# Performance work log

Hardware: AMD Instinct MI355X
Metric: run time of the kernel (lower is better)

Reference implementation:

```python
import jax, jax.numpy as jnp
import numpy as np

B, T, S, D, V = 32, 2048, 256, 1024, 56
STAR_PENALTY = -1.0
NEG = -1e30  # -inf surrogate that is safe for gradients


def setup_inputs() -> dict:
    key = jax.random.key(0)
    k1, k2, k3 = jax.random.split(key, 3)
    features = jax.random.normal(k1, (B, T, D), jnp.float32)
    targets = jax.random.randint(k2, (B, S), 1, V)  # 0 is the blank; labels in [1, V)
    W = jax.random.normal(k3, (V, D), jnp.float32) * (1.0 / 32.0)  # 1/sqrt(D)
    b = jnp.zeros((V,), jnp.float32)
    input_lengths = jnp.full((B,), T, jnp.int32)
    target_lengths = jnp.full((B,), S, jnp.int32)
    return dict(features=features, W=W, b=b, targets=targets,
                input_lengths=input_lengths, target_lengths=target_lengths)


def _star_ctc_losses(logp, targets, input_lengths, target_lengths, star_penalty):
    """Star-CTC forward (DP) score.
    logp: (T, N, C) log-softmax emissions; targets: (N, S) labels (blank=0 excluded).
    Extended state sequence [*, t1, *, t2, ..., tS, *]: star states play the role of
    CTC blanks but act as penalized wildcards, emitting logsumexp(logp)+star_penalty
    (== star_penalty for normalized log-probs). Standard CTC transition topology:
    self-loop, advance by 1, advance by 2 into a token state when it differs from the
    previous token. Returns per-sequence negative log-likelihood, shape (N,)."""
    Tlen, N, C = logp.shape
    Slen = targets.shape[1]
    L = 2 * Slen + 1
    ext = jnp.zeros((N, L), targets.dtype).at[:, 1::2].set(targets)  # (N, L)
    is_star = (jnp.arange(L) % 2 == 0)[None, :]                      # (1, L)
    prev2 = jnp.pad(ext[:, :-2], ((0, 0), (2, 0)), constant_values=-1)
    allow_skip = (~is_star) & (ext != prev2)                         # (N, L)

    def emit(logp_t):  # logp_t: (N, C) -> (N, L)
        star_e = star_penalty + jax.nn.logsumexp(logp_t, axis=-1, keepdims=True)
        tok_e = jnp.take_along_axis(logp_t, ext, axis=-1)
        return jnp.where(is_star, star_e, tok_e)

    alpha0 = jnp.where(jnp.arange(L)[None, :] < 2, emit(logp[0]), NEG)

    def step(alpha, xs):
        logp_t, t = xs
        a1 = jnp.pad(alpha[:, :-1], ((0, 0), (1, 0)), constant_values=NEG)
        a2 = jnp.where(allow_skip,
                       jnp.pad(alpha[:, :-2], ((0, 0), (2, 0)), constant_values=NEG),
                       NEG)
        new = jnp.logaddexp(jnp.logaddexp(alpha, a1), a2) + emit(logp_t)
        new = jnp.where(t < input_lengths[:, None], new, alpha)  # freeze past input_length
        return new, None

    alpha, _ = jax.lax.scan(step, alpha0, (logp[1:], jnp.arange(1, Tlen)))
    last = 2 * target_lengths                  # index of the final star state
    rows = jnp.arange(N)
    score = jnp.logaddexp(alpha[rows, last], alpha[rows, last - 1])
    return -score


def reference(features, W, b, targets, input_lengths, target_lengths):
    # classifier + log_softmax (Dropout(0.2) is identity at eval time)
    logits = jnp.einsum('btd,vd->btv', features, W) + b
    logp = jax.nn.log_softmax(logits.astype(jnp.float32), axis=-1)
    logp = jnp.transpose(logp, (1, 0, 2))      # (T, N, C) as in logits.permute(1,0,2)
    losses = _star_ctc_losses(logp, targets, input_lengths, target_lengths, STAR_PENALTY)
    # ctc_reduce_mean: length-normalized mean loss
    return jnp.mean(losses / target_lengths.astype(losses.dtype))
```

## Files before the change

### kernel.cpp

```cpp
#include <hip/hip_runtime.h>
#include <hip/hip_bf16.h>
#include <math.h>

typedef __attribute__((ext_vector_type(4))) float f32x4;
typedef __attribute__((ext_vector_type(8))) short s16x8;

#define LOG2E 1.4426950408889634f
#define LN2f  0.6931471805599453f
#define INV_E 0.36787944117144233f

__device__ __forceinline__ short bfc(float x) {
  unsigned u = __float_as_uint(x);
  unsigned r = u + 0x7fffu + ((u >> 16) & 1u);
  return (short)(r >> 16);
}

__device__ __forceinline__ unsigned pk2(float x, float y) {
  union { __hip_bfloat162 h; unsigned u; } c;
  c.h = __float22bfloat162_rn(make_float2(x, y));
  return c.u;
}

__device__ __forceinline__ float bperm(float v, int byte_addr) {
  return __int_as_float(__builtin_amdgcn_ds_bpermute(byte_addr, __float_as_int(v)));
}

__device__ __forceinline__ float rdlane(float v, int lane) {
  return __int_as_float(__builtin_amdgcn_readlane(__float_as_int(v), lane));
}

__device__ __forceinline__ float pick9(int j, float a0, float a1, float a2,
                                       float a3, float a4, float a5, float a6,
                                       float a7, float a8) {
  float v = a0;
  if (j == 1) v = a1;
  if (j == 2) v = a2;
  if (j == 3) v = a3;
  if (j == 4) v = a4;
  if (j == 5) v = a5;
  if (j == 6) v = a6;
  if (j == 7) v = a7;
  if (j == 8) v = a8;
  return v;
}

__global__ void conv_w(const float* __restrict__ W, short* __restrict__ Wb,
                       int V, int D) {
  int idx = blockIdx.x * blockDim.x + threadIdx.x;
  if (idx >= 64 * D) return;
  int row = idx / D, col = idx - row * D;
  Wb[idx] = (row < V) ? bfc(W[(size_t)row * D + col]) : (short)0;
}

__global__ __launch_bounds__(256) void fused_gemm_star(
    const float* __restrict__ feat, const short* __restrict__ Wb,
    const float* __restrict__ bias, float* __restrict__ pt,
    int* __restrict__ flags,
    const int* __restrict__ targets, const int* __restrict__ in_len,
    const int* __restrict__ tgt_len, float* __restrict__ partial,
    int nrows, int D, int V, int T, int S, int B, int CPB) {

  if ((int)blockIdx.x >= B) {
    const int j = blockIdx.x - B;
    const int b = j % B;
    const int c = j / B;
    const int tc0 = c * 128;
    const int rlen = (T - tc0 < 128) ? (T - tc0) : 128;
    const int rowlim = b * T + tc0 + rlen;

    const int lane = threadIdx.x & 63;
    const int wave = threadIdx.x >> 6;
    const int m_lo = lane & 15;
    const int q = lane >> 4;
    const int rowbase = b * T + tc0 + wave * 32;

    int arow0 = rowbase + m_lo;
    int arow1 = rowbase + 16 + m_lo;
    if (arow0 >= nrows) arow0 = nrows - 1;
    if (arow1 >= nrows) arow1 = nrows - 1;
    const float* Ap0 = feat + (size_t)arow0 * D + q * 8;
    const float* Ap1 = feat + (size_t)arow1 * D + q * 8;
    const short* Bp = Wb + (size_t)m_lo * D + q * 8;
    const size_t bstr = (size_t)16 * D;

    f32x4 acc[2][4];
    #pragma unroll
    for (int g = 0; g < 2; ++g)
      #pragma unroll
      for (int ni = 0; ni < 4; ++ni) acc[g][ni] = (f32x4){0.f, 0.f, 0.f, 0.f};

    float4 al0 = *(const float4*)(Ap0);
    float4 ah0 = *(const float4*)(Ap0 + 4);
    float4 al1 = *(const float4*)(Ap1);
    float4 ah1 = *(const float4*)(Ap1 + 4);
    s16x8 b0 = *(const s16x8*)(Bp);
    s16x8 b1 = *(const s16x8*)(Bp + bstr);
    s16x8 b2 = *(const s16x8*)(Bp + 2 * bstr);
    s16x8 b3 = *(const s16x8*)(Bp + 3 * bstr);

    for (int k0 = 0; k0 < D; k0 += 32) {
      const int kn = (k0 + 32 < D) ? (k0 + 32) : 0;
      const float* Ap0n = feat + (size_t)arow0 * D + kn + q * 8;
      const float* Ap1n = feat + (size_t)arow1 * D + kn + q * 8;
      const short* Bpn = Wb + (size_t)m_lo * D + kn + q * 8;
      float4 nal0 = *(const float4*)(Ap0n);
      float4 nah0 = *(const float4*)(Ap0n + 4);
      float4 nal1 = *(const float4*)(Ap1n);
      float4 nah1 = *(const float4*)(Ap1n + 4);
      s16x8 nb0 = *(const s16x8*)(Bpn);
      s16x8 nb1 = *(const s16x8*)(Bpn + bstr);
      s16x8 nb2 = *(const s16x8*)(Bpn + 2 * bstr);
      s16x8 nb3 = *(const s16x8*)(Bpn + 3 * bstr);

      union { s16x8 v; unsigned u[4]; } av0, av1;
      av0.u[0] = pk2(al0.x, al0.y); av0.u[1] = pk2(al0.z, al0.w);
      av0.u[2] = pk2(ah0.x, ah0.y); av0.u[3] = pk2(ah0.z, ah0.w);
      av1.u[0] = pk2(al1.x, al1.y); av1.u[1] = pk2(al1.z, al1.w);
      av1.u[2] = pk2(ah1.x, ah1.y); av1.u[3] = pk2(ah1.z, ah1.w);

      acc[0][0] = __builtin_amdgcn_mfma_f32_16x16x32_bf16(av0.v, b0, acc[0][0], 0, 0, 0);
      acc[0][1] = __builtin_amdgcn_mfma_f32_16x16x32_bf16(av0.v, b1, acc[0][1], 0, 0, 0);
      acc[0][2] = __builtin_amdgcn_mfma_f32_16x16x32_bf16(av0.v, b2, acc[0][2], 0, 0, 0);
      acc[0][3] = __builtin_amdgcn_mfma_f32_16x16x32_bf16(av0.v, b3, acc[0][3], 0, 0, 0);
      acc[1][0] = __builtin_amdgcn_mfma_f32_16x16x32_bf16(av1.v, b0, acc[1][0], 0, 0, 0);
      acc[1][1] = __builtin_amdgcn_mfma_f32_16x16x32_bf16(av1.v, b1, acc[1][1], 0, 0, 0);
      acc[1][2] = __builtin_amdgcn_mfma_f32_16x16x32_bf16(av1.v, b2, acc[1][2], 0, 0, 0);
      acc[1][3] = __builtin_amdgcn_mfma_f32_16x16x32_bf16(av1.v, b3, acc[1][3], 0, 0, 0);

      al0 = nal0; ah0 = nah0; al1 = nal1; ah1 = nah1;
      b0 = nb0; b1 = nb1; b2 = nb2; b3 = nb3;
    }

    float bias_v[4];
    #pragma unroll
    for (int ni = 0; ni < 4; ++ni) {
      int col = ni * 16 + m_lo;
      bias_v[ni] = (col < V) ? bias[col] : 0.f;
    }

    #pragma unroll
    for (int g = 0; g < 2; ++g) {
      #pragma unroll
      for (int r = 0; r < 4; ++r) {
        int grow = rowbase + g * 16 + q * 4 + r;
        float lg[4];
        #pragma unroll
        for (int ni = 0; ni < 4; ++ni) {
          int col = ni * 16 + m_lo;
          lg[ni] = (col < V) ? (acc[g][ni][r] + bias_v[ni]) : -1e30f;
        }
        float m = fmaxf(fmaxf(lg[0], lg[1]), fmaxf(lg[2], lg[3]));
        #pragma unroll
        for (int off = 1; off < 16; off <<= 1) m = fmaxf(m, __shfl_xor(m, off));
        float p[4];
        #pragma unroll
        for (int ni = 0; ni < 4; ++ni) p[ni] = exp2f((lg[ni] - m) * LOG2E);
        float s = (p[0] + p[1]) + (p[2] + p[3]);
        #pragma unroll
        for (int off = 1; off < 16; off <<= 1) s += __shfl_xor(s, off);

        if (grow < rowlim) {
          float* orow = pt + (size_t)grow * 64;
          orow[m_lo] = p[0];
          orow[16 + m_lo] = p[1];
          orow[32 + m_lo] = p[2];
          if (m_lo < 8)       orow[48 + m_lo] = p[3];
          else if (m_lo == 8) orow[56] = logf(s);
          else if (m_lo == 9) orow[57] = s * INV_E;
          else                orow[48 + m_lo] = 0.f;
        }
      }
    }

    __syncthreads();
    if (threadIdx.x == 0)
      __hip_atomic_store(&flags[b * CPB + c], 1, __ATOMIC_RELEASE,
                         __HIP_MEMORY_SCOPE_AGENT);
    return;
  }

  if (threadIdx.x >= 64) return;
  const int n = blockIdx.x;
  const int lane = threadIdx.x;
  const float* row = pt + (size_t)n * T * 64;
  const int len = in_len[n];
  const int tl = tgt_len[n];
  const int* tg = targets + (size_t)n * S;
  const int* fl = flags + n * CPB;

  int cdone = -1;
#define WAITC(cc)                                                            \
  do {                                                                       \
    int _c = (cc);                                                           \
    while (cdone < _c) {                                                     \
      if (__hip_atomic_load((int*)&fl[cdone + 1], __ATOMIC_ACQUIRE,          \
                            __HIP_MEMORY_SCOPE_AGENT))                       \
        ++cdone;                                                             \
      else                                                                   \
        __builtin_amdgcn_s_sleep(2);                                         \
    }                                                                        \
  } while (0)

  const int s0 = lane * 4;
  int lab1 = (s0     < S) ? tg[s0]     : 0;
  int lab3 = (s0 + 1 < S) ? tg[s0 + 1] : 0;
  int lab5 = (s0 + 2 < S) ? tg[s0 + 2] : 0;
  int lab7 = (s0 + 3 < S) ? tg[s0 + 3] : 0;
  int labm1 = __shfl_up(lab7, 1);
  int labm3 = __shfl_up(lab5, 1);
  const bool sk1 = (lane > 0) && (lab1 != labm1);
  const bool sk3 = (lab3 != lab1);
  const bool sk5 = (lab5 != lab3);
  const bool sk7 = (lab7 != lab5);
  const bool skm1 = (labm1 != labm3);
  const int ad1 = lab1 << 2, ad3 = lab3 << 2, ad5 = lab5 << 2, ad7 = lab7 << 2;
  const int adm1 = labm1 << 2;

  float a0 = 0, a1 = 0, a2 = 0, a3 = 0, a4 = 0, a5 = 0, a6 = 0, a7 = 0, a8 = 0;
  float m1 = 0.f, m2 = 0.f, m3 = 0.f;
  int eps = 0, eL = 0;
  bool act = (lane == 0);

#define ROWL(t) row[(size_t)(((t) < len) ? (t) : (len - 1)) * 64 + lane]

  WAITC(0);

  float rc = row[lane];
  {
    float star = rdlane(rc, 57);
    float e1i = bperm(rc, ad1);
    if (lane == 0) { a0 = star; a1 = e1i; }
  }
  float ksum = rc;

  float rr0 = ROWL(1), rr1 = ROWL(2), rr2 = ROWL(3), rr3 = ROWL(4);
  float rr4 = ROWL(5), rr5 = ROWL(6), rr6 = ROWL(7), rr7 = ROWL(8);

  float es0v = rdlane(rr0, 57);
  float e1a = bperm(rr0, ad1), e3a = bperm(rr0, ad3);
  float e5a = bperm(rr0, ad5), e7a = bperm(rr0, ad7);
  float em1a = bperm(rr0, adm1);
  float es1v = rdlane(rr1, 57);
  float e1b = bperm(rr1, ad1), e3b = bperm(rr1, ad3);
  float e5b = bperm(rr1, ad5), e7b = bperm(rr1, ad7);

#define RENORM()                                                             \
  do {                                                                       \
    float mx = fmaxf(fmaxf(fmaxf(a0, a1), fmaxf(a2, a3)),                    \
                     fmaxf(fmaxf(a4, a5), fmaxf(a6, a7)));                   \
    mx = fmaxf(mx, a8);                                                      \
    int e = (int)((__float_as_uint(mx) >> 23) & 255) - 126;                  \
    e = (act && mx > 0.f) ? e : 0;                                           \
    a0 = ldexpf(a0, -e); a1 = ldexpf(a1, -e); a2 = ldexpf(a2, -e);           \
    a3 = ldexpf(a3, -e); a4 = ldexpf(a4, -e); a5 = ldexpf(a5, -e);           \
    a6 = ldexpf(a6, -e); a7 = ldexpf(a7, -e); a8 = ldexpf(a8, -e);           \
    eps += e;                                                                \
  } while (0)

#define PAIR(C0, C1, N0, N1, P0, P1, DOREN)                                  \
  do {                                                                       \
    ksum += C0; ksum += C1;                                                  \
    if (!act) eps = eL;                                                      \
    bool inc = (lane != 0) &&                                                \
               ((m1 != 0.f) || (m2 != 0.f) || (m3 != 0.f));                  \
    int d = inc ? (eL - eps) : 0;                                            \
    if (__builtin_expect(d > 24, 0)) {                  \
      a0 = ldexpf(a0, -d); a1 = ldexpf(a1, -d); a2 = ldexpf(a2, -d);         \
      a3 = ldexpf(a3, -d); a4 = ldexpf(a4, -d); a5 = ldexpf(a5, -d);         \
      a6 = ldexpf(a6, -d); a7 = ldexpf(a7, -d); a8 = ldexpf(a8, -d);         \
      eps += d;                                      \
    } else {                                                                 \
      m1 = ldexpf(m1, d); m2 = ldexpf(m2, d); m3 = ldexpf(m3, d);            \
    }                                                                        \
    act = act || (m1 != 0.f) || (m2 != 0.f) || (m3 != 0.f);                  \
                  \
    a8 = (a8 + a7) * es0v;                                                   \
    a7 = (a7 + a6 + (sk7 ? a5 : 0.f)) * e7a;                                 \
    a6 = (a6 + a5) * es0v;                                                   \
    a5 = (a5 + a4 + (sk5 ? a3 : 0.f)) * e5a;                                 \
    a4 = (a4 + a3) * es0v;                                                   \
    a3 = (a3 + a2 + (sk3 ? a1 : 0.f)) * e3a;                                 \
    a2 = (a2 + a1) * es0v;                                                   \
    a1 = (a1 + a0 + (sk1 ? m1 : 0.f)) * e1a;                                 \
    a0 = (a0 + m1) * es0v;                                                   \
    m1 = (m1 + m2 + (skm1 ? m3 : 0.f)) * em1a;                               \
                                                             \
    a8 = (a8 + a7) * es1v;                                                   \
    a7 = (a7 + a6 + (sk7 ? a5 : 0.f)) * e7b;                                 \
    a6 = (a6 + a5) * es1v;                                                   \
    a5 = (a5 + a4 + (sk5 ? a3 : 0.f)) * e5b;                                 \
    a4 = (a4 + a3) * es1v;                                                   \
    a3 = (a3 + a2 + (sk3 ? a1 : 0.f)) * e3b;                                 \
    a2 = (a2 + a1) * es1v;                                                   \
    a1 = (a1 + a0 + (sk1 ? m1 : 0.f)) * e1b;                                 \
    a0 = (a0 + m1) * es1v;                                                   \
    C0 = ROWL(P0); C1 = ROWL(P1);                     \
    if (DOREN) RENORM();                                                     \
      \
    es0v = rdlane(N0, 57);                                                   \
    e1a = bperm(N0, ad1); e3a = bperm(N0, ad3);                              \
    e5a = bperm(N0, ad5); e7a = bperm(N0, ad7);                              \
    em1a = bperm(N0, adm1);                                                  \
    es1v = rdlane(N1, 57);                                                   \
    e1b = bperm(N1, ad1); e3b = bperm(N1, ad3);                              \
    e5b = bperm(N1, ad5); e7b = bperm(N1, ad7);                              \
                          \
    m3 = __shfl_up(a5, 1); m2 = __shfl_up(a6, 1); m1 = __shfl_up(a7, 1);     \
    eL = __shfl_up(eps, 1);                                                  \
    if (lane == 0) { m1 = 0.f; m2 = 0.f; m3 = 0.f; }                         \
  } while (0)

  int t0 = 1;
  for (; t0 + 8 <= len; t0 += 8) {
    int tmax = t0 + 15;
    if (tmax > len - 1) tmax = len - 1;
    WAITC(tmax >> 7);
    PAIR(rr0, rr1, rr2, rr3, t0 + 8,  t0 + 9,  false);
    PAIR(rr2, rr3, rr4, rr5, t0 + 10, t0 + 11, false);
    PAIR(rr4, rr5, rr6, rr7, t0 + 12, t0 + 13, false);
    PAIR(rr6, rr7, rr0, rr1, t0 + 14, t0 + 15, true);
  }

  WAITC((len - 1) >> 7);

  for (int t = t0; t < len; ++t) {
    float cur = ROWL(t);
    float esv = rdlane(cur, 57);
    float e1v = bperm(cur, ad1), e3v = bperm(cur, ad3);
    float e5v = bperm(cur, ad5), e7v = bperm(cur, ad7);
    ksum += cur;
    if (!act) eps = eL;
    bool inc = (lane != 0) && (m1 != 0.f);
    int d = inc ? (eL - eps) : 0;
    float m1s;
    if (__builtin_expect(d > 24, 0)) {
      a0 = ldexpf(a0, -d); a1 = ldexpf(a1, -d); a2 = ldexpf(a2, -d);
      a3 = ldexpf(a3, -d); a4 = ldexpf(a4, -d); a5 = ldexpf(a5, -d);
      a6 = ldexpf(a6, -d); a7 = ldexpf(a7, -d); a8 = ldexpf(a8, -d);
      eps += d; m1s = m1;
    } else {
      m1s = inc ? ldexpf(m1, d) : 0.f;
    }
    act = act || (m1s != 0.f);
    a8 = (a8 + a7) * esv;
    a7 = (a7 + a6 + (sk7 ? a5 : 0.f)) * e7v;
    a6 = (a6 + a5) * esv;
    a5 = (a5 + a4 + (sk5 ? a3 : 0.f)) * e5v;
    a4 = (a4 + a3) * esv;
    a3 = (a3 + a2 + (sk3 ? a1 : 0.f)) * e3v;
    a2 = (a2 + a1) * esv;
    a1 = (a1 + a0 + (sk1 ? m1s : 0.f)) * e1v;
    a0 = (a0 + m1s) * esv;
    if ((t & 7) == 0) RENORM();
    m1 = __shfl_up(a7, 1);
    eL = __shfl_up(eps, 1);
    if (lane == 0) m1 = 0.f;
  }

  int last = 2 * tl;
  int kx = last >> 3, jx = last & 7;
  if (kx > 63) { kx = 63; jx = last - 504; }
  int ky = (last - 1) >> 3, jy = (last - 1) & 7;
  float vx = pick9(jx, a0, a1, a2, a3, a4, a5, a6, a7, a8);
  float vy = pick9(jy, a0, a1, a2, a3, a4, a5, a6, a7, a8);
  float k56 = __shfl(ksum, 56);
  float sx = __shfl(vx, kx); int ex = __shfl(eps, kx);
  float sy = __shfl(vy, ky); int ey = __shfl(eps, ky);
  if (lane == 0) {
    int em = (ex > ey) ? ex : ey;
    float v = ldexpf(sx, ex - em) + ldexpf(sy, ey - em);
    float score = logf(v) + (float)em * LN2f - k56;
    partial[n] = -score / (float)tl;
  }
#undef WAITC
#undef ROWL
#undef RENORM
#undef PAIR
}

__global__ void reduce_mean(const float* __restrict__ partial,
                            float* __restrict__ out, int B) {
  float v = 0.f;
  for (int i = threadIdx.x; i < B; i += 64) v += partial[i];
  #pragma unroll
  for (int off = 32; off > 0; off >>= 1) v += __shfl_down(v, off, 64);
  if (threadIdx.x == 0) out[0] = v / (float)B;
}

extern "C" void kernel_launch(void* const* d_in, const int* in_sizes, int n_in,
                              void* d_out, int out_size, void* d_ws, size_t ws_size,
                              hipStream_t stream) {
  const float* feat = (const float*)d_in[0];
  const float* W = (const float*)d_in[1];
  const float* bias = (const float*)d_in[2];
  const int* targets = (const int*)d_in[3];
  const int* in_len = (const int*)d_in[4];
  const int* tgt_len = (const int*)d_in[5];
  float* out = (float*)d_out;

  const int V = in_sizes[2];
  const int D = in_sizes[1] / V;
  const int B = in_sizes[4];
  const int T = in_sizes[0] / (B * D);
  const int S = in_sizes[3] / B;
  const int nrows = B * T;

  float* pt = (float*)d_ws;
  float* partial = pt + (size_t)nrows * 64;
  short* Wb = (short*)(partial + B);
  const int CPB = (T + 127) / 128;
  int* flags = (int*)((char*)Wb + (size_t)64 * D * sizeof(short));

  hipMemsetAsync(flags, 0, (size_t)B * CPB * sizeof(int), stream);

  conv_w<<<(64 * D + 255) / 256, 256, 0, stream>>>(W, Wb, V, D);

  fused_gemm_star<<<dim3(B + B * CPB), 256, 0, stream>>>(
      feat, Wb, bias, pt, flags, targets, in_len, tgt_len, partial,
      nrows, D, V, T, S, B, CPB);

  reduce_mean<<<1, 64, 0, stream>>>(partial, out, B);
}
```

Before: 754.8 us.

## Pre-gather per-lane target emissions in producer blocks and persist producer grid

Producer blocks now gather, for each time row, the four token emissions each consumer lane needs (indexed by that lane's target labels) into a float4-per-lane buffer. The star emission and log-sum go into a separate small buffer. This removes the ds_bpermute and readlane work from the serial DP consumer loop, which is latency-bound. Producers become a persistent grid of up to 256-B blocks that loop over tiles in time-chunk-major order. Flag polling now uses a relaxed load with a single acquire fence. The cost is a 4x larger emission buffer written to global memory plus extra LDS traffic in the epilogue.

```diff
diff --git a/kernel.cpp b/kernel.cpp
--- a/kernel.cpp
+++ b/kernel.cpp
@@ -19,10 +19,6 @@
   union { __hip_bfloat162 h; unsigned u; } c;
   c.h = __float22bfloat162_rn(make_float2(x, y));
   return c.u;
-}
-
-__device__ __forceinline__ float bperm(float v, int byte_addr) {
-  return __int_as_float(__builtin_amdgcn_ds_bpermute(byte_addr, __float_as_int(v)));
 }
 
 __device__ __forceinline__ float rdlane(float v, int lane) {
@@ -54,150 +50,178 @@
 
 __global__ __launch_bounds__(256) void fused_gemm_star(
     const float* __restrict__ feat, const short* __restrict__ Wb,
-    const float* __restrict__ bias, float* __restrict__ pt,
-    int* __restrict__ flags,
+    const float* __restrict__ bias, float* __restrict__ ptg,
+    float* __restrict__ skb, int* __restrict__ flags,
     const int* __restrict__ targets, const int* __restrict__ in_len,
     const int* __restrict__ tgt_len, float* __restrict__ partial,
     int nrows, int D, int V, int T, int S, int B, int CPB) {
 
+  __shared__ float gbuf[4][4][64];
+
   if ((int)blockIdx.x >= B) {
-    const int j = blockIdx.x - B;
-    const int b = j % B;
-    const int c = j / B;
-    const int tc0 = c * 128;
-    const int rlen = (T - tc0 < 128) ? (T - tc0) : 128;
-    const int rowlim = b * T + tc0 + rlen;
-
+    const int NPROD = gridDim.x - B;
+    const int NTILES = B * CPB;
     const int lane = threadIdx.x & 63;
     const int wave = threadIdx.x >> 6;
     const int m_lo = lane & 15;
     const int q = lane >> 4;
-    const int rowbase = b * T + tc0 + wave * 32;
-
-    int arow0 = rowbase + m_lo;
-    int arow1 = rowbase + 16 + m_lo;
-    if (arow0 >= nrows) arow0 = nrows - 1;
-    if (arow1 >= nrows) arow1 = nrows - 1;
-    const float* Ap0 = feat + (size_t)arow0 * D + q * 8;
-    const float* Ap1 = feat + (size_t)arow1 * D + q * 8;
-    const short* Bp = Wb + (size_t)m_lo * D + q * 8;
     const size_t bstr = (size_t)16 * D;
 
-    f32x4 acc[2][4];
-    #pragma unroll
-    for (int g = 0; g < 2; ++g)
+    for (int i = blockIdx.x - B; i < NTILES; i += NPROD) {
+      const int c = i / B;
+      const int b = i - c * B;
+      const int tc0 = c * 128;
+      const int rlen = (T - tc0 < 128) ? (T - tc0) : 128;
+      const int rowlim = b * T + tc0 + rlen;
+      const int rowbase = b * T + tc0 + wave * 32;
+
+      const int* tg = targets + (size_t)b * S;
+      const int l0 = lane * 4;
+      const int g1 = (l0 < S) ? tg[l0] : 0;
+      const int g3 = (l0 + 1 < S) ? tg[l0 + 1] : 0;
+      const int g5 = (l0 + 2 < S) ? tg[l0 + 2] : 0;
+      const int g7 = (l0 + 3 < S) ? tg[l0 + 3] : 0;
+
+      int arow0 = rowbase + m_lo;
+      int arow1 = rowbase + 16 + m_lo;
+      if (arow0 >= nrows) arow0 = nrows - 1;
+      if (arow1 >= nrows) arow1 = nrows - 1;
+      const short* Bp = Wb + (size_t)m_lo * D + q * 8;
+
+      f32x4 acc[2][4];
       #pragma unroll
-      for (int ni = 0; ni < 4; ++ni) acc[g][ni] = (f32x4){0.f, 0.f, 0.f, 0.f};
-
-    float4 al0 = *(const float4*)(Ap0);
-    float4 ah0 = *(const float4*)(Ap0 + 4);
-    float4 al1 = *(const float4*)(Ap1);
-    float4 ah1 = *(const float4*)(Ap1 + 4);
-    s16x8 b0 = *(const s16x8*)(Bp);
-    s16x8 b1 = *(const s16x8*)(Bp + bstr);
-    s16x8 b2 = *(const s16x8*)(Bp + 2 * bstr);
-    s16x8 b3 = *(const s16x8*)(Bp + 3 * bstr);
-
-    for (int k0 = 0; k0 < D; k0 += 32) {
-      const int kn = (k0 + 32 < D) ? (k0 + 32) : 0;
-      const float* Ap0n = feat + (size_t)arow0 * D + kn + q * 8;
-      const float* Ap1n = feat + (size_t)arow1 * D + kn + q * 8;
-      const short* Bpn = Wb + (size_t)m_lo * D + kn + q * 8;
-      float4 nal0 = *(const float4*)(Ap0n);
-      float4 nah0 = *(const float4*)(Ap0n + 4);
-      float4 nal1 = *(const float4*)(Ap1n);
-      float4 nah1 = *(const float4*)(Ap1n + 4);
-      s16x8 nb0 = *(const s16x8*)(Bpn);
-      s16x8 nb1 = *(const s16x8*)(Bpn + bstr);
-      s16x8 nb2 = *(const s16x8*)(Bpn + 2 * bstr);
-      s16x8 nb3 = *(const s16x8*)(Bpn + 3 * bstr);
-
-      union { s16x8 v; unsigned u[4]; } av0, av1;
-      av0.u[0] = pk2(al0.x, al0.y); av0.u[1] = pk2(al0.z, al0.w);
-      av0.u[2] = pk2(ah0.x, ah0.y); av0.u[3] = pk2(ah0.z, ah0.w);
-      av1.u[0] = pk2(al1.x, al1.y); av1.u[1] = pk2(al1.z, al1.w);
-      av1.u[2] = pk2(ah1.x, ah1.y); av1.u[3] = pk2(ah1.z, ah1.w);
-
-      acc[0][0] = __builtin_amdgcn_mfma_f32_16x16x32_bf16(av0.v, b0, acc[0][0], 0, 0, 0);
-      acc[0][1] = __builtin_amdgcn_mfma_f32_16x16x32_bf16(av0.v, b1, acc[0][1], 0, 0, 0);
-      acc[0][2] = __builtin_amdgcn_mfma_f32_16x16x32_bf16(av0.v, b2, acc[0][2], 0, 0, 0);
-      acc[0][3] = __builtin_amdgcn_mfma_f32_16x16x32_bf16(av0.v, b3, acc[0][3], 0, 0, 0);
-      acc[1][0] = __builtin_amdgcn_mfma_f32_16x16x32_bf16(av1.v, b0, acc[1][0], 0, 0, 0);
-      acc[1][1] = __builtin_amdgcn_mfma_f32_16x16x32_bf16(av1.v, b1, acc[1][1], 0, 0, 0);
-      acc[1][2] = __builtin_amdgcn_mfma_f32_16x16x32_bf16(av1.v, b2, acc[1][2], 0, 0, 0);
-      acc[1][3] = __builtin_amdgcn_mfma_f32_16x16x32_bf16(av1.v, b3, acc[1][3], 0, 0, 0);
-
-      al0 = nal0; ah0 = nah0; al1 = nal1; ah1 = nah1;
-      b0 = nb0; b1 = nb1; b2 = nb2; b3 = nb3;
-    }
-
-    float bias_v[4];
-    #pragma unroll
-    for (int ni = 0; ni < 4; ++ni) {
-      int col = ni * 16 + m_lo;
-      bias_v[ni] = (col < V) ? bias[col] : 0.f;
-    }
-
-    #pragma unroll
-    for (int g = 0; g < 2; ++g) {
+      for (int g = 0; g < 2; ++g)
+        #pragma unroll
+        for (int ni = 0; ni < 4; ++ni) acc[g][ni] = (f32x4){0.f, 0.f, 0.f, 0.f};
+
+      const float* Ap0 = feat + (size_t)arow0 * D + q * 8;
+      const float* Ap1 = feat + (size_t)arow1 * D + q * 8;
+      float4 al0 = *(const float4*)(Ap0);
+      float4 ah0 = *(const float4*)(Ap0 + 4);
+      float4 al1 = *(const float4*)(Ap1);
+      float4 ah1 = *(const float4*)(Ap1 + 4);
+      s16x8 b0 = *(const s16x8*)(Bp);
+      s16x8 b1 = *(const s16x8*)(Bp + bstr);
+      s16x8 b2 = *(const s16x8*)(Bp + 2 * bstr);
+      s16x8 b3 = *(const s16x8*)(Bp + 3 * bstr);
+
+      for (int k0 = 0; k0 < D; k0 += 32) {
+        const int kn = (k0 + 32 < D) ? (k0 + 32) : 0;
+        const float* Ap0n = feat + (size_t)arow0 * D + kn + q * 8;
+        const float* Ap1n = feat + (size_t)arow1 * D + kn + q * 8;
+        const short* Bpn = Wb + (size_t)m_lo * D + kn + q * 8;
+        float4 nal0 = *(const float4*)(Ap0n);
+        float4 nah0 = *(const float4*)(Ap0n + 4);
+        float4 nal1 = *(const float4*)(Ap1n);
+        float4 nah1 = *(const float4*)(Ap1n + 4);
+        s16x8 nb0 = *(const s16x8*)(Bpn);
+        s16x8 nb1 = *(const s16x8*)(Bpn + bstr);
+        s16x8 nb2 = *(const s16x8*)(Bpn + 2 * bstr);
+        s16x8 nb3 = *(const s16x8*)(Bpn + 3 * bstr);
+
+        union { s16x8 v; unsigned u[4]; } av0, av1;
+        av0.u[0] = pk2(al0.x, al0.y); av0.u[1] = pk2(al0.z, al0.w);
+        av0.u[2] = pk2(ah0.x, ah0.y); av0.u[3] = pk2(ah0.z, ah0.w);
+        av1.u[0] = pk2(al1.x, al1.y); av1.u[1] = pk2(al1.z, al1.w);
+        av1.u[2] = pk2(ah1.x, ah1.y); av1.u[3] = pk2(ah1.z, ah1.w);
+
+        acc[0][0] = __builtin_amdgcn_mfma_f32_16x16x32_bf16(av0.v, b0, acc[0][0], 0, 0, 0);
+        acc[0][1] = __builtin_amdgcn_mfma_f32_16x16x32_bf16(av0.v, b1, acc[0][1], 0, 0, 0);
+        acc[0][2] = __builtin_amdgcn_mfma_f32_16x16x32_bf16(av0.v, b2, acc[0][2], 0, 0, 0);
+        acc[0][3] = __builtin_amdgcn_mfma_f32_16x16x32_bf16(av0.v, b3, acc[0][3], 0, 0, 0);
+        acc[1][0] = __builtin_amdgcn_mfma_f32_16x16x32_bf16(av1.v, b0, acc[1][0], 0, 0, 0);
+        acc[1][1] = __builtin_amdgcn_mfma_f32_16x16x32_bf16(av1.v, b1, acc[1][1], 0, 0, 0);
+        acc[1][2] = __builtin_amdgcn_mfma_f32_16x16x32_bf16(av1.v, b2, acc[1][2], 0, 0, 0);
+        acc[1][3] = __builtin_amdgcn_mfma_f32_16x16x32_bf16(av1.v, b3, acc[1][3], 0, 0, 0);
+
+        al0 = nal0; ah0 = nah0; al1 = nal1; ah1 = nah1;
+        b0 = nb0; b1 = nb1; b2 = nb2; b3 = nb3;
+      }
+
+      float bias_v[4];
       #pragma unroll
-      for (int r = 0; r < 4; ++r) {
-        int grow = rowbase + g * 16 + q * 4 + r;
-        float lg[4];
+      for (int ni = 0; ni < 4; ++ni) {
+        int col = ni * 16 + m_lo;
+        bias_v[ni] = (col < V) ? bias[col] : 0.f;
+      }
+
+      #pragma unroll
+      for (int g = 0; g < 2; ++g) {
         #pragma unroll
-        for (int ni = 0; ni < 4; ++ni) {
-          int col = ni * 16 + m_lo;
-          lg[ni] = (col < V) ? (acc[g][ni][r] + bias_v[ni]) : -1e30f;
-        }
-        float m = fmaxf(fmaxf(lg[0], lg[1]), fmaxf(lg[2], lg[3]));
-        #pragma unroll
-        for (int off = 1; off < 16; off <<= 1) m = fmaxf(m, __shfl_xor(m, off));
-        float p[4];
-        #pragma unroll
-        for (int ni = 0; ni < 4; ++ni) p[ni] = exp2f((lg[ni] - m) * LOG2E);
-        float s = (p[0] + p[1]) + (p[2] + p[3]);
-        #pragma unroll
-        for (int off = 1; off < 16; off <<= 1) s += __shfl_xor(s, off);
-
-        if (grow < rowlim) {
-          float* orow = pt + (size_t)grow * 64;
-          orow[m_lo] = p[0];
-          orow[16 + m_lo] = p[1];
-          orow[32 + m_lo] = p[2];
-          if (m_lo < 8)       orow[48 + m_lo] = p[3];
-          else if (m_lo == 8) orow[56] = logf(s);
-          else if (m_lo == 9) orow[57] = s * INV_E;
-          else                orow[48 + m_lo] = 0.f;
+        for (int r = 0; r < 4; ++r) {
+          float lg[4];
+          #pragma unroll
+          for (int ni = 0; ni < 4; ++ni) {
+            int col = ni * 16 + m_lo;
+            lg[ni] = (col < V) ? (acc[g][ni][r] + bias_v[ni]) : -1e30f;
+          }
+          float m = fmaxf(fmaxf(lg[0], lg[1]), fmaxf(lg[2], lg[3]));
+          #pragma unroll
+          for (int off = 1; off < 16; off <<= 1) m = fmaxf(m, __shfl_xor(m, off));
+          float p[4];
+          #pragma unroll
+          for (int ni = 0; ni < 4; ++ni) p[ni] = exp2f((lg[ni] - m) * LOG2E);
+          float s = (p[0] + p[1]) + (p[2] + p[3]);
+          #pragma unroll
+          for (int off = 1; off < 16; off <<= 1) s += __shfl_xor(s, off);
+
+          #pragma unroll
+          for (int ni = 0; ni < 4; ++ni)
+            gbuf[wave][q][ni * 16 + m_lo] = p[ni];
+
+          #pragma unroll
+          for (int rr = 0; rr < 4; ++rr) {
+            int grow = rowbase + g * 16 + rr * 4 + r;
+            if (grow < rowlim) {
+              float srow = rdlane(s, rr * 16);
+              float4 ev;
+              ev.x = gbuf[wave][rr][g1];
+              ev.y = gbuf[wave][rr][g3];
+              ev.z = gbuf[wave][rr][g5];
+              ev.w = gbuf[wave][rr][g7];
+              *(float4*)(ptg + ((size_t)grow * 64 + lane) * 4) = ev;
+              if (lane == 0) {
+                float2 skv;
+                skv.x = srow * INV_E;
+                skv.y = logf(srow);
+                *(float2*)(skb + (size_t)grow * 2) = skv;
+              }
+            }
+          }
         }
       }
+
+      __syncthreads();
+      if (threadIdx.x == 0)
+        __hip_atomic_store(&flags[b * CPB + c], 1, __ATOMIC_RELEASE,
+                           __HIP_MEMORY_SCOPE_AGENT);
     }
-
-    __syncthreads();
-    if (threadIdx.x == 0)
-      __hip_atomic_store(&flags[b * CPB + c], 1, __ATOMIC_RELEASE,
-                         __HIP_MEMORY_SCOPE_AGENT);
     return;
   }
 
   if (threadIdx.x >= 64) return;
   const int n = blockIdx.x;
   const int lane = threadIdx.x;
-  const float* row = pt + (size_t)n * T * 64;
   const int len = in_len[n];
   const int tl = tgt_len[n];
   const int* tg = targets + (size_t)n * S;
   const int* fl = flags + n * CPB;
+  const float* prow = ptg + (size_t)n * T * 256;
+  const float* srow = skb + (size_t)n * T * 2;
 
   int cdone = -1;
 #define WAITC(cc)                                                            \
   do {                                                                       \
     int _c = (cc);                                                           \
-    while (cdone < _c) {                                                     \
-      if (__hip_atomic_load((int*)&fl[cdone + 1], __ATOMIC_ACQUIRE,          \
-                            __HIP_MEMORY_SCOPE_AGENT))                       \
-        ++cdone;                                                             \
-      else                                                                   \
-        __builtin_amdgcn_s_sleep(2);                                         \
+    if (cdone < _c) {                                                        \
+      while (cdone < _c) {                                                   \
+        if (__hip_atomic_load((int*)&fl[cdone + 1], __ATOMIC_RELAXED,        \
+                              __HIP_MEMORY_SCOPE_AGENT))                     \
+          ++cdone;                                                           \
+        else                                                                 \
+          __builtin_amdgcn_s_sleep(8);                                       \
+      }                                                                      \
+      __builtin_amdgcn_fence(__ATOMIC_ACQUIRE, "agent");                     \
     }                                                                        \
   } while (0)
 
@@ -213,36 +237,30 @@
   const bool sk5 = (lab5 != lab3);
   const bool sk7 = (lab7 != lab5);
   const bool skm1 = (labm1 != labm3);
-  const int ad1 = lab1 << 2, ad3 = lab3 << 2, ad5 = lab5 << 2, ad7 = lab7 << 2;
-  const int adm1 = labm1 << 2;
 
   float a0 = 0, a1 = 0, a2 = 0, a3 = 0, a4 = 0, a5 = 0, a6 = 0, a7 = 0, a8 = 0;
   float m1 = 0.f, m2 = 0.f, m3 = 0.f;
   int eps = 0, eL = 0;
   bool act = (lane == 0);
 
-#define ROWL(t) row[(size_t)(((t) < len) ? (t) : (len - 1)) * 64 + lane]
+#define PTGL(t) (*(const float4*)(prow +                                     \
+    ((size_t)(((t) < len) ? (t) : (len - 1)) * 256 + lane * 4)))
+#define SKLL(t) (*(const float2*)(srow +                                     \
+    ((size_t)(((t) < len) ? (t) : (len - 1)) * 2)))
 
   WAITC(0);
 
-  float rc = row[lane];
-  {
-    float star = rdlane(rc, 57);
-    float e1i = bperm(rc, ad1);
-    if (lane == 0) { a0 = star; a1 = e1i; }
-  }
-  float ksum = rc;
-
-  float rr0 = ROWL(1), rr1 = ROWL(2), rr2 = ROWL(3), rr3 = ROWL(4);
-  float rr4 = ROWL(5), rr5 = ROWL(6), rr6 = ROWL(7), rr7 = ROWL(8);
-
-  float es0v = rdlane(rr0, 57);
-  float e1a = bperm(rr0, ad1), e3a = bperm(rr0, ad3);
-  float e5a = bperm(rr0, ad5), e7a = bperm(rr0, ad7);
-  float em1a = bperm(rr0, adm1);
-  float es1v = rdlane(rr1, 57);
-  float e1b = bperm(rr1, ad1), e3b = bperm(rr1, ad3);
-  float e5b = bperm(rr1, ad5), e7b = bperm(rr1, ad7);
+  float4 r0 = PTGL(0);
+  float2 k0v = SKLL(0);
+  if (lane == 0) { a0 = k0v.x; a1 = r0.x; }
+  float ksum = k0v.y;
+
+  float4 rr0 = PTGL(1), rr1 = PTGL(2), rr2 = PTGL(3), rr3 = PTGL(4);
+  float4 rr4 = PTGL(5), rr5 = PTGL(6), rr6 = PTGL(7), rr7 = PTGL(8);
+  float2 kr0 = SKLL(1), kr1 = SKLL(2), kr2 = SKLL(3), kr3 = SKLL(4);
+  float2 kr4 = SKLL(5), kr5 = SKLL(6), kr6 = SKLL(7), kr7 = SKLL(8);
+
+  float em1a = __shfl_up(rr0.w, 1);
 
 #define RENORM()                                                             \
   do {                                                                       \
@@ -257,9 +275,9 @@
     eps += e;                                                                \
   } while (0)
 
-#define PAIR(C0, C1, N0, N1, P0, P1, DOREN)                                  \
+#define PAIR(EC0, EC1, KC0, KC1, NX, P0, P1, DOREN)                          \
   do {                                                                       \
-    ksum += C0; ksum += C1;                                                  \
+    ksum += KC0.y; ksum += KC1.y;                                            \
     if (!act) eps = eL;                                                      \
     bool inc = (lane != 0) &&                                                \
                ((m1 != 0.f) || (m2 != 0.f) || (m3 != 0.f));                  \
@@ -274,36 +292,30 @@
     }                                                                        \
     act = act || (m1 != 0.f) || (m2 != 0.f) || (m3 != 0.f);                  \
                   \
-    a8 = (a8 + a7) * es0v;                                                   \
-    a7 = (a7 + a6 + (sk7 ? a5 : 0.f)) * e7a;                                 \
-    a6 = (a6 + a5) * es0v;                                                   \
-    a5 = (a5 + a4 + (sk5 ? a3 : 0.f)) * e5a;                                 \
-    a4 = (a4 + a3) * es0v;                                                   \
-    a3 = (a3 + a2 + (sk3 ? a1 : 0.f)) * e3a;                                 \
-    a2 = (a2 + a1) * es0v;                                                   \
-    a1 = (a1 + a0 + (sk1 ? m1 : 0.f)) * e1a;                                 \
-    a0 = (a0 + m1) * es0v;                                                   \
+    a8 = (a8 + a7) * KC0.x;                                                  \
+    a7 = (a7 + a6 + (sk7 ? a5 : 0.f)) * EC0.w;                               \
+    a6 = (a6 + a5) * KC0.x;                                                  \
+    a5 = (a5 + a4 + (sk5 ? a3 : 0.f)) * EC0.z;                               \
+    a4 = (a4 + a3) * KC0.x;                                                  \
+    a3 = (a3 + a2 + (sk3 ? a1 : 0.f)) * EC0.y;                               \
+    a2 = (a2 + a1) * KC0.x;                                                  \
+    a1 = (a1 + a0 + (sk1 ? m1 : 0.f)) * EC0.x;                               \
+    a0 = (a0 + m1) * KC0.x;                                                  \
     m1 = (m1 + m2 + (skm1 ? m3 : 0.f)) * em1a;                               \
                                                              \
-    a8 = (a8 + a7) * es1v;                                                   \
-    a7 = (a7 + a6 + (sk7 ? a5 : 0.f)) * e7b;                                 \
-    a6 = (a6 + a5) * es1v;                                                   \
-    a5 = (a5 + a4 + (sk5 ? a3 : 0.f)) * e5b;                                 \
-    a4 = (a4 + a3) * es1v;                                                   \
-    a3 = (a3 + a2 + (sk3 ? a1 : 0.f)) * e3b;                                 \
-    a2 = (a2 + a1) * es1v;                                                   \
-    a1 = (a1 + a0 + (sk1 ? m1 : 0.f)) * e1b;                                 \
-    a0 = (a0 + m1) * es1v;                                                   \
-    C0 = ROWL(P0); C1 = ROWL(P1);                     \
+    a8 = (a8 + a7) * KC1.x;                                                  \
+    a7 = (a7 + a6 + (sk7 ? a5 : 0.f)) * EC1.w;                               \
+    a6 = (a6 + a5) * KC1.x;                                                  \
+    a5 = (a5 + a4 + (sk5 ? a3 : 0.f)) * EC1.z;                               \
+    a4 = (a4 + a3) * KC1.x;                                                  \
+    a3 = (a3 + a2 + (sk3 ? a1 : 0.f)) * EC1.y;                               \
+    a2 = (a2 + a1) * KC1.x;                                                  \
+    a1 = (a1 + a0 + (sk1 ? m1 : 0.f)) * EC1.x;                               \
+    a0 = (a0 + m1) * KC1.x;                                                  \
+    EC0 = PTGL(P0); EC1 = PTGL(P1);                   \
+    KC0 = SKLL(P0); KC1 = SKLL(P1);                                          \
     if (DOREN) RENORM();                                                     \
-      \
-    es0v = rdlane(N0, 57);                                                   \
-    e1a = bperm(N0, ad1); e3a = bperm(N0, ad3);                              \
-    e5a = bperm(N0, ad5); e7a = bperm(N0, ad7);                              \
-    em1a = bperm(N0, adm1);                                                  \
-    es1v = rdlane(N1, 57);                                                   \
-    e1b = bperm(N1, ad1); e3b = bperm(N1, ad3);                              \
-    e5b = bperm(N1, ad5); e7b = bperm(N1, ad7);                              \
+    em1a = __shfl_up(NX.w, 1);                     \
                           \
     m3 = __shfl_up(a5, 1); m2 = __shfl_up(a6, 1); m1 = __shfl_up(a7, 1);     \
     eL = __shfl_up(eps, 1);                                                  \
@@ -315,20 +327,18 @@
     int tmax = t0 + 15;
     if (tmax > len - 1) tmax = len - 1;
     WAITC(tmax >> 7);
-    PAIR(rr0, rr1, rr2, rr3, t0 + 8,  t0 + 9,  false);
-    PAIR(rr2, rr3, rr4, rr5, t0 + 10, t0 + 11, false);
-    PAIR(rr4, rr5, rr6, rr7, t0 + 12, t0 + 13, false);
-    PAIR(rr6, rr7, rr0, rr1, t0 + 14, t0 + 15, true);
+    PAIR(rr0, rr1, kr0, kr1, rr2, t0 + 8,  t0 + 9,  false);
+    PAIR(rr2, rr3, kr2, kr3, rr4, t0 + 10, t0 + 11, false);
+    PAIR(rr4, rr5, kr4, kr5, rr6, t0 + 12, t0 + 13, false);
+    PAIR(rr6, rr7, kr6, kr7, rr0, t0 + 14, t0 + 15, true);
   }
 
   WAITC((len - 1) >> 7);
 
   for (int t = t0; t < len; ++t) {
-    float cur = ROWL(t);
-    float esv = rdlane(cur, 57);
-    float e1v = bperm(cur, ad1), e3v = bperm(cur, ad3);
-    float e5v = bperm(cur, ad5), e7v = bperm(cur, ad7);
-    ksum += cur;
+    float4 cv = PTGL(t);
+    float2 kc = SKLL(t);
+    ksum += kc.y;
     if (!act) eps = eL;
     bool inc = (lane != 0) && (m1 != 0.f);
     int d = inc ? (eL - eps) : 0;
@@ -342,15 +352,15 @@
       m1s = inc ? ldexpf(m1, d) : 0.f;
     }
     act = act || (m1s != 0.f);
-    a8 = (a8 + a7) * esv;
-    a7 = (a7 + a6 + (sk7 ? a5 : 0.f)) * e7v;
-    a6 = (a6 + a5) * esv;
-    a5 = (a5 + a4 + (sk5 ? a3 : 0.f)) * e5v;
-    a4 = (a4 + a3) * esv;
-    a3 = (a3 + a2 + (sk3 ? a1 : 0.f)) * e3v;
-    a2 = (a2 + a1) * esv;
-    a1 = (a1 + a0 + (sk1 ? m1s : 0.f)) * e1v;
-    a0 = (a0 + m1s) * esv;
+    a8 = (a8 + a7) * kc.x;
+    a7 = (a7 + a6 + (sk7 ? a5 : 0.f)) * cv.w;
+    a6 = (a6 + a5) * kc.x;
+    a5 = (a5 + a4 + (sk5 ? a3 : 0.f)) * cv.z;
+    a4 = (a4 + a3) * kc.x;
+    a3 = (a3 + a2 + (sk3 ? a1 : 0.f)) * cv.y;
+    a2 = (a2 + a1) * kc.x;
+    a1 = (a1 + a0 + (sk1 ? m1s : 0.f)) * cv.x;
+    a0 = (a0 + m1s) * kc.x;
     if ((t & 7) == 0) RENORM();
     m1 = __shfl_up(a7, 1);
     eL = __shfl_up(eps, 1);
@@ -363,17 +373,17 @@
   int ky = (last - 1) >> 3, jy = (last - 1) & 7;
   float vx = pick9(jx, a0, a1, a2, a3, a4, a5, a6, a7, a8);
   float vy = pick9(jy, a0, a1, a2, a3, a4, a5, a6, a7, a8);
-  float k56 = __shfl(ksum, 56);
   float sx = __shfl(vx, kx); int ex = __shfl(eps, kx);
   float sy = __shfl(vy, ky); int ey = __shfl(eps, ky);
   if (lane == 0) {
     int em = (ex > ey) ? ex : ey;
     float v = ldexpf(sx, ex - em) + ldexpf(sy, ey - em);
-    float score = logf(v) + (float)em * LN2f - k56;
+    float score = logf(v) + (float)em * LN2f - ksum;
     partial[n] = -score / (float)tl;
   }
 #undef WAITC
-#undef ROWL
+#undef PTGL
+#undef SKLL
 #undef RENORM
 #undef PAIR
 }
@@ -405,8 +415,9 @@
   const int S = in_sizes[3] / B;
   const int nrows = B * T;
 
-  float* pt = (float*)d_ws;
-  float* partial = pt + (size_t)nrows * 64;
+  float* ptg = (float*)d_ws;
+  float* skb = ptg + (size_t)nrows * 256;
+  float* partial = skb + (size_t)nrows * 2;
   short* Wb = (short*)(partial + B);
   const int CPB = (T + 127) / 128;
   int* flags = (int*)((char*)Wb + (size_t)64 * D * sizeof(short));
@@ -415,8 +426,11 @@
 
   conv_w<<<(64 * D + 255) / 256, 256, 0, stream>>>(W, Wb, V, D);
 
-  fused_gemm_star<<<dim3(B + B * CPB), 256, 0, stream>>>(
-      feat, Wb, bias, pt, flags, targets, in_len, tgt_len, partial,
+  int NPROD = 256 - B;
+  const int NTILES = B * CPB;
+  if (NPROD > NTILES) NPROD = NTILES;
+  fused_gemm_star<<<dim3(B + NPROD), 256, 0, stream>>>(
+      feat, Wb, bias, ptg, skb, flags, targets, in_len, tgt_len, partial,
       nrows, D, V, T, S, B, CPB);
 
   reduce_mean<<<1, 64, 0, stream>>>(partial, out, B);
```

Measured after the change: 721.2 us. -4.5%, faster.

## Stage feature tiles through swizzled LDS with persistent producer blocks

Applied to the files above, without the earlier changes.

Producer blocks become persistent, with 128 looping over the tiles in chunk-major order instead of one block per tile. Each wave stages its 32x128 fp32 feature panel into LDS via global_load_lds with an XOR swizzle, then reads MFMA A operands from LDS. Flag zeroing moves into conv_w so the memset launch goes away, and the consumer spin-wait uses relaxed loads followed by one acquire fence. The swizzled direct-to-LDS loads aim for better coalescing and fewer launches. The cost is that the register prefetch pipelining is lost: the LDS panel waits on vmcnt(0) with no double buffering, and there are fewer producer blocks.

```diff
diff --git a/kernel.cpp b/kernel.cpp
--- a/kernel.cpp
+++ b/kernel.cpp
@@ -44,9 +44,16 @@
   return v;
 }
 
+__device__ __forceinline__ void gload_lds16(const float* g, float* l) {
+  __builtin_amdgcn_global_load_lds(
+      (const __attribute__((address_space(1))) unsigned int*)g,
+      (__attribute__((address_space(3))) unsigned int*)l, 16, 0, 0);
+}
+
 __global__ void conv_w(const float* __restrict__ W, short* __restrict__ Wb,
-                       int V, int D) {
+                       int V, int D, int* __restrict__ flags, int nflags) {
   int idx = blockIdx.x * blockDim.x + threadIdx.x;
+  if (idx < nflags) flags[idx] = 0;
   if (idx >= 64 * D) return;
   int row = idx / D, col = idx - row * D;
   Wb[idx] = (row < V) ? bfc(W[(size_t)row * D + col]) : (short)0;
@@ -60,122 +67,122 @@
     const int* __restrict__ tgt_len, float* __restrict__ partial,
     int nrows, int D, int V, int T, int S, int B, int CPB) {
 
+  __shared__ __align__(16) float Ap[4 * 32 * 128];
+
   if ((int)blockIdx.x >= B) {
-    const int j = blockIdx.x - B;
-    const int b = j % B;
-    const int c = j / B;
-    const int tc0 = c * 128;
-    const int rlen = (T - tc0 < 128) ? (T - tc0) : 128;
-    const int rowlim = b * T + tc0 + rlen;
-
+    const int NPROD = gridDim.x - B;
+    const int NTILES = B * CPB;
     const int lane = threadIdx.x & 63;
     const int wave = threadIdx.x >> 6;
     const int m_lo = lane & 15;
     const int q = lane >> 4;
-    const int rowbase = b * T + tc0 + wave * 32;
-
-    int arow0 = rowbase + m_lo;
-    int arow1 = rowbase + 16 + m_lo;
-    if (arow0 >= nrows) arow0 = nrows - 1;
-    if (arow1 >= nrows) arow1 = nrows - 1;
-    const float* Ap0 = feat + (size_t)arow0 * D + q * 8;
-    const float* Ap1 = feat + (size_t)arow1 * D + q * 8;
-    const short* Bp = Wb + (size_t)m_lo * D + q * 8;
-    const size_t bstr = (size_t)16 * D;
-
-    f32x4 acc[2][4];
-    #pragma unroll
-    for (int g = 0; g < 2; ++g)
+    float* wpan = Ap + wave * 32 * 128;
+    char* wpanb = (char*)wpan;
+
+    for (int i = blockIdx.x - B; i < NTILES; i += NPROD) {
+      const int c = i / B;
+      const int b = i - c * B;
+      const int tc0 = c * 128;
+      const int rlen = (T - tc0 < 128) ? (T - tc0) : 128;
+      const int rowlim = b * T + tc0 + rlen;
+      const int rowbase = b * T + tc0 + wave * 32;
+
+      f32x4 acc[2][4];
       #pragma unroll
-      for (int ni = 0; ni < 4; ++ni) acc[g][ni] = (f32x4){0.f, 0.f, 0.f, 0.f};
-
-    float4 al0 = *(const float4*)(Ap0);
-    float4 ah0 = *(const float4*)(Ap0 + 4);
-    float4 al1 = *(const float4*)(Ap1);
-    float4 ah1 = *(const float4*)(Ap1 + 4);
-    s16x8 b0 = *(const s16x8*)(Bp);
-    s16x8 b1 = *(const s16x8*)(Bp + bstr);
-    s16x8 b2 = *(const s16x8*)(Bp + 2 * bstr);
-    s16x8 b3 = *(const s16x8*)(Bp + 3 * bstr);
-
-    for (int k0 = 0; k0 < D; k0 += 32) {
-      const int kn = (k0 + 32 < D) ? (k0 + 32) : 0;
-      const float* Ap0n = feat + (size_t)arow0 * D + kn + q * 8;
-      const float* Ap1n = feat + (size_t)arow1 * D + kn + q * 8;
-      const short* Bpn = Wb + (size_t)m_lo * D + kn + q * 8;
-      float4 nal0 = *(const float4*)(Ap0n);
-      float4 nah0 = *(const float4*)(Ap0n + 4);
-      float4 nal1 = *(const float4*)(Ap1n);
-      float4 nah1 = *(const float4*)(Ap1n + 4);
-      s16x8 nb0 = *(const s16x8*)(Bpn);
-      s16x8 nb1 = *(const s16x8*)(Bpn + bstr);
-      s16x8 nb2 = *(const s16x8*)(Bpn + 2 * bstr);
-      s16x8 nb3 = *(const s16x8*)(Bpn + 3 * bstr);
-
-      union { s16x8 v; unsigned u[4]; } av0, av1;
-      av0.u[0] = pk2(al0.x, al0.y); av0.u[1] = pk2(al0.z, al0.w);
-      av0.u[2] = pk2(ah0.x, ah0.y); av0.u[3] = pk2(ah0.z, ah0.w);
-      av1.u[0] = pk2(al1.x, al1.y); av1.u[1] = pk2(al1.z, al1.w);
-      av1.u[2] = pk2(ah1.x, ah1.y); av1.u[3] = pk2(ah1.z, ah1.w);
-
-      acc[0][0] = __builtin_amdgcn_mfma_f32_16x16x32_bf16(av0.v, b0, acc[0][0], 0, 0, 0);
-      acc[0][1] = __builtin_amdgcn_mfma_f32_16x16x32_bf16(av0.v, b1, acc[0][1], 0, 0, 0);
-      acc[0][2] = __builtin_amdgcn_mfma_f32_16x16x32_bf16(av0.v, b2, acc[0][2], 0, 0, 0);
-      acc[0][3] = __builtin_amdgcn_mfma_f32_16x16x32_bf16(av0.v, b3, acc[0][3], 0, 0, 0);
-      acc[1][0] = __builtin_amdgcn_mfma_f32_16x16x32_bf16(av1.v, b0, acc[1][0], 0, 0, 0);
-      acc[1][1] = __builtin_amdgcn_mfma_f32_16x16x32_bf16(av1.v, b1, acc[1][1], 0, 0, 0);
-      acc[1][2] = __builtin_amdgcn_mfma_f32_16x16x32_bf16(av1.v, b2, acc[1][2], 0, 0, 0);
-      acc[1][3] = __builtin_amdgcn_mfma_f32_16x16x32_bf16(av1.v, b3, acc[1][3], 0, 0, 0);
-
-      al0 = nal0; ah0 = nah0; al1 = nal1; ah1 = nah1;
-      b0 = nb0; b1 = nb1; b2 = nb2; b3 = nb3;
-    }
-
-    float bias_v[4];
-    #pragma unroll
-    for (int ni = 0; ni < 4; ++ni) {
-      int col = ni * 16 + m_lo;
-      bias_v[ni] = (col < V) ? bias[col] : 0.f;
-    }
-
-    #pragma unroll
-    for (int g = 0; g < 2; ++g) {
-      #pragma unroll
-      for (int r = 0; r < 4; ++r) {
-        int grow = rowbase + g * 16 + q * 4 + r;
-        float lg[4];
+      for (int g = 0; g < 2; ++g)
         #pragma unroll
-        for (int ni = 0; ni < 4; ++ni) {
-          int col = ni * 16 + m_lo;
-          lg[ni] = (col < V) ? (acc[g][ni][r] + bias_v[ni]) : -1e30f;
+        for (int ni = 0; ni < 4; ++ni) acc[g][ni] = (f32x4){0.f, 0.f, 0.f, 0.f};
+
+      const int xl = (lane & 31) * 16;
+      const int rhalf = lane >> 5;
+
+      for (int k0 = 0; k0 < D; k0 += 128) {
+        #pragma unroll
+        for (int ii = 0; ii < 16; ++ii) {
+          int rl = ii * 2 + rhalf;
+          int grow = rowbase + rl;
+          if (grow >= nrows) grow = nrows - 1;
+          int off = xl ^ ((rl & 7) << 4);
+          gload_lds16(feat + (size_t)grow * D + k0 + (off >> 2),
+                      wpan + ii * 256);
         }
-        float m = fmaxf(fmaxf(lg[0], lg[1]), fmaxf(lg[2], lg[3]));
+        asm volatile("s_waitcnt vmcnt(0)" ::: "memory");
+        const int l0 = m_lo, l1 = m_lo + 16;
+        const int sz0 = (l0 & 7) << 4;
         #pragma unroll
-        for (int off = 1; off < 16; off <<= 1) m = fmaxf(m, __shfl_xor(m, off));
-        float p[4];
-        #pragma unroll
-        for (int ni = 0; ni < 4; ++ni) p[ni] = exp2f((lg[ni] - m) * LOG2E);
-        float s = (p[0] + p[1]) + (p[2] + p[3]);
-        #pragma unroll
-        for (int off = 1; off < 16; off <<= 1) s += __shfl_xor(s, off);
-
-        if (grow < rowlim) {
-          float* orow = pt + (size_t)grow * 64;
-          orow[m_lo] = p[0];
-          orow[16 + m_lo] = p[1];
-          orow[32 + m_lo] = p[2];
-          if (m_lo < 8)       orow[48 + m_lo] = p[3];
-          else if (m_lo == 8) orow[56] = logf(s);
-          else if (m_lo == 9) orow[57] = s * INV_E;
-          else                orow[48 + m_lo] = 0.f;
+        for (int kk = 0; kk < 4; ++kk) {
+          int boff = kk * 128 + q * 32;
+          float4 lo0 = *(const float4*)(wpanb + l0 * 512 + ((boff) ^ sz0));
+          float4 hi0 = *(const float4*)(wpanb + l0 * 512 + ((boff + 16) ^ sz0));
+          float4 lo1 = *(const float4*)(wpanb + l1 * 512 + ((boff) ^ sz0));
+          float4 hi1 = *(const float4*)(wpanb + l1 * 512 + ((boff + 16) ^ sz0));
+          const short* Bpp = Wb + (size_t)m_lo * D + k0 + kk * 32 + q * 8;
+          s16x8 b0 = *(const s16x8*)(Bpp);
+          s16x8 b1 = *(const s16x8*)(Bpp + (size_t)16 * D);
+          s16x8 b2 = *(const s16x8*)(Bpp + (size_t)32 * D);
+          s16x8 b3 = *(const s16x8*)(Bpp + (size_t)48 * D);
+          union { s16x8 v; unsigned u[4]; } av0, av1;
+          av0.u[0] = pk2(lo0.x, lo0.y); av0.u[1] = pk2(lo0.z, lo0.w);
+          av0.u[2] = pk2(hi0.x, hi0.y); av0.u[3] = pk2(hi0.z, hi0.w);
+          av1.u[0] = pk2(lo1.x, lo1.y); av1.u[1] = pk2(lo1.z, lo1.w);
+          av1.u[2] = pk2(hi1.x, hi1.y); av1.u[3] = pk2(hi1.z, hi1.w);
+          acc[0][0] = __builtin_amdgcn_mfma_f32_16x16x32_bf16(av0.v, b0, acc[0][0], 0, 0, 0);
+          acc[0][1] = __builtin_amdgcn_mfma_f32_16x16x32_bf16(av0.v, b1, acc[0][1], 0, 0, 0);
+          acc[0][2] = __builtin_amdgcn_mfma_f32_16x16x32_bf16(av0.v, b2, acc[0][2], 0, 0, 0);
+          acc[0][3] = __builtin_amdgcn_mfma_f32_16x16x32_bf16(av0.v, b3, acc[0][3], 0, 0, 0);
+          acc[1][0] = __builtin_amdgcn_mfma_f32_16x16x32_bf16(av1.v, b0, acc[1][0], 0, 0, 0);
+          acc[1][1] = __builtin_amdgcn_mfma_f32_16x16x32_bf16(av1.v, b1, acc[1][1], 0, 0, 0);
+          acc[1][2] = __builtin_amdgcn_mfma_f32_16x16x32_bf16(av1.v, b2, acc[1][2], 0, 0, 0);
+          acc[1][3] = __builtin_amdgcn_mfma_f32_16x16x32_bf16(av1.v, b3, acc[1][3], 0, 0, 0);
         }
       }
+
+      float bias_v[4];
+      #pragma unroll
+      for (int ni = 0; ni < 4; ++ni) {
+        int col = ni * 16 + m_lo;
+        bias_v[ni] = (col < V) ? bias[col] : 0.f;
+      }
+
+      #pragma unroll
+      for (int g = 0; g < 2; ++g) {
+        #pragma unroll
+        for (int r = 0; r < 4; ++r) {
+          int grow = rowbase + g * 16 + q * 4 + r;
+          float lg[4];
+          #pragma unroll
+          for (int ni = 0; ni < 4; ++ni) {
+            int col = ni * 16 + m_lo;
+            lg[ni] = (col < V) ? (acc[g][ni][r] + bias_v[ni]) : -1e30f;
+          }
+          float m = fmaxf(fmaxf(lg[0], lg[1]), fmaxf(lg[2], lg[3]));
+          #pragma unroll
+          for (int off = 1; off < 16; off <<= 1) m = fmaxf(m, __shfl_xor(m, off));
+          float p[4];
+          #pragma unroll
+          for (int ni = 0; ni < 4; ++ni) p[ni] = exp2f((lg[ni] - m) * LOG2E);
+          float s = (p[0] + p[1]) + (p[2] + p[3]);
+          #pragma unroll
+          for (int off = 1; off < 16; off <<= 1) s += __shfl_xor(s, off);
+
+          if (grow < rowlim) {
+            float* orow = pt + (size_t)grow * 64;
+            orow[m_lo] = p[0];
+            orow[16 + m_lo] = p[1];
+            orow[32 + m_lo] = p[2];
+            if (m_lo < 8)       orow[48 + m_lo] = p[3];
+            else if (m_lo == 8) orow[56] = logf(s);
+            else if (m_lo == 9) orow[57] = s * INV_E;
+            else                orow[48 + m_lo] = 0.f;
+          }
+        }
+      }
+
+      __syncthreads();
+      if (threadIdx.x == 0)
+        __hip_atomic_store(&flags[b * CPB + c], 1, __ATOMIC_RELEASE,
+                           __HIP_MEMORY_SCOPE_AGENT);
     }
-
-    __syncthreads();
-    if (threadIdx.x == 0)
-      __hip_atomic_store(&flags[b * CPB + c], 1, __ATOMIC_RELEASE,
-                         __HIP_MEMORY_SCOPE_AGENT);
     return;
   }
 
@@ -192,12 +199,15 @@
 #define WAITC(cc)                                                            \
   do {                                                                       \
     int _c = (cc);                                                           \
-    while (cdone < _c) {                                                     \
-      if (__hip_atomic_load((int*)&fl[cdone + 1], __ATOMIC_ACQUIRE,          \
-                            __HIP_MEMORY_SCOPE_AGENT))                       \
-        ++cdone;                                                             \
-      else                                                                   \
-        __builtin_amdgcn_s_sleep(2);                                         \
+    if (cdone < _c) {                                                        \
+      while (cdone < _c) {                                                   \
+        if (__hip_atomic_load((int*)&fl[cdone + 1], __ATOMIC_RELAXED,        \
+                              __HIP_MEMORY_SCOPE_AGENT))                     \
+          ++cdone;                                                           \
+        else                                                                 \
+          __builtin_amdgcn_s_sleep(2);                                       \
+      }                                                                      \
+      __builtin_amdgcn_fence(__ATOMIC_ACQUIRE, "agent");                     \
     }                                                                        \
   } while (0)
 
@@ -411,11 +421,13 @@
   const int CPB = (T + 127) / 128;
   int* flags = (int*)((char*)Wb + (size_t)64 * D * sizeof(short));
 
-  hipMemsetAsync(flags, 0, (size_t)B * CPB * sizeof(int), stream);
-
-  conv_w<<<(64 * D + 255) / 256, 256, 0, stream>>>(W, Wb, V, D);
-
-  fused_gemm_star<<<dim3(B + B * CPB), 256, 0, stream>>>(
+  conv_w<<<(64 * D + 255) / 256, 256, 0, stream>>>(W, Wb, V, D,
+                                                   flags, B * CPB);
+
+  const int NTILES = B * CPB;
+  int NPROD = 128;
+  if (NPROD > NTILES) NPROD = NTILES;
+  fused_gemm_star<<<dim3(B + NPROD), 256, 0, stream>>>(
       feat, Wb, bias, pt, flags, targets, in_len, tgt_len, partial,
       nrows, D, V, T, S, B, CPB);
 
```

Result: faster. 670.7 us (-11.1%).
